# Kernel optimization log

Measured on AMD Instinct MI355X. Metric: run time of the kernel, lower is better.

The kernel has to match this reference:

```python
import jax, jax.numpy as jnp
import numpy as np


def setup_inputs() -> dict:
    key = jax.random.key(0)
    k1, k2, k3 = jax.random.split(key, 3)
    B, H, G, L, S, D = 2, 8, 4, 2048, 2048, 128
    q = jax.random.normal(k1, (B, H, G, L, D), dtype=jnp.float32)
    k = jax.random.normal(k2, (B, H, 1, S, D), dtype=jnp.float32)
    v = jax.random.normal(k3, (B, H, 1, S, D), dtype=jnp.float32)
    return {"q": q, "k": k, "v": v}


def reference(q, k, v):
    # q: [B,H,G,L,D]; k,v: [B,H,1,S,D] broadcast over G groups.
    # NOTE: original module does NOT scale by 1/sqrt(D).
    kk = jnp.squeeze(k, axis=2)  # [B,H,S,D]
    vv = jnp.squeeze(v, axis=2)  # [B,H,S,D]
    scores = jnp.einsum('bhgld,bhsd->bhgls', q, kk)  # [B,H,G,L,S]
    probs = jax.nn.softmax(scores, axis=-1)
    return jnp.einsum('bhgls,bhsd->bhgld', probs, vv)  # [B,H,G,L,D]
```

## Files before the change

kernel.cpp:

```cpp
#include <hip/hip_runtime.h>
#include <hip/hip_bf16.h>
#include <math.h>

typedef __bf16 bf16x8 __attribute__((ext_vector_type(8)));
typedef __bf16 bf16x4 __attribute__((ext_vector_type(4)));
typedef float  f32x4  __attribute__((ext_vector_type(4)));

constexpr int D   = 128;
constexpr int LQ  = 2048;
constexpr int SK  = 2048;
constexpr int BM  = 256;
constexpr int BN  = 64;
constexpr int NKV = 16;

__device__ __forceinline__ void load_lds16(const void* g, void* l) {
  __builtin_amdgcn_global_load_lds((const __attribute__((address_space(1))) unsigned*)g,
                                   (__attribute__((address_space(3))) unsigned*)l, 16, 0, 0);
}

__global__ __launch_bounds__(256) void conv_k(const float* __restrict__ k,
                                              __bf16* __restrict__ khi,
                                              __bf16* __restrict__ klo) {
  const size_t i = ((size_t)blockIdx.x * 256 + threadIdx.x) * 4;
  f32x4 a = *(const f32x4*)(k + i);
  bf16x4 hi, lo;
#pragma unroll
  for (int j = 0; j < 4; ++j) {
    hi[j] = (__bf16)a[j];
    lo[j] = (__bf16)(a[j] - (float)hi[j]);
  }
  *(bf16x4*)(khi + i) = hi;
  *(bf16x4*)(klo + i) = lo;
}

__global__ __launch_bounds__(256) void transpose_v(const float* __restrict__ v,
                                                   __bf16* __restrict__ vt) {
  const int b    = blockIdx.x;
  const int bh   = b >> 6;
  const int blk2 = b & 63;
  const int t    = threadIdx.x;
  const int s0   = (blk2 * 2 + (t >> 7)) * 16;
  const int d    = t & 127;
  const float* src = v + ((size_t)bh * SK + s0) * D + d;
  bf16x8 o0, o1;
#pragma unroll
  for (int j = 0; j < 8; ++j) o0[j] = (__bf16)src[j * D];
#pragma unroll
  for (int j = 0; j < 8; ++j) o1[j] = (__bf16)src[(8 + j) * D];
  __bf16* dst = vt + ((size_t)bh * D + d) * SK + s0;
  *(bf16x8*)dst = o0;
  *(bf16x8*)(dst + 8) = o1;
}

__global__ __launch_bounds__(512, 2)
void gqa_fwd(const float* __restrict__ qg, const __bf16* __restrict__ khi_g,
             const __bf16* __restrict__ klo_g, const __bf16* __restrict__ vt_g,
             float* __restrict__ outg)
{
  __shared__ alignas(16) __bf16 Kh[2][BN * D];
  __shared__ alignas(16) __bf16 Kl[2][BN * D];
  __shared__ alignas(16) __bf16 Vs[2][D * BN];

  const int bid   = blockIdx.x;
  const int xcd   = bid & 7;
  const int idx   = bid >> 3;
  const int bh    = 2 * xcd + (idx & 1);
  const int grp   = (idx >> 1) & 3;
  const int qtile = idx >> 3;
  const int bhg   = bh * 4 + grp;

  const int tid  = threadIdx.x;
  const int wave = tid >> 6;
  const int lane = tid & 63;
  const int i16  = lane & 15;
  const int quad = lane >> 4;

  const float*  qbase = qg + (size_t)bhg * (LQ * D) + (size_t)(qtile * BM) * D;
  const __bf16* khb   = khi_g + (size_t)bh * (SK * D);
  const __bf16* klb   = klo_g + (size_t)bh * (SK * D);
  const __bf16* vtb   = vt_g + (size_t)bh * (D * SK);

  auto stage = [&](int s0, int buf) {
#pragma unroll
    for (int c = 0; c < 2; ++c) {
      const int wc   = 2 * wave + c;
      const int srow = wc * 4 + (lane >> 4);
      const int jk   = (lane & 15) ^ (srow & 15);
      load_lds16(khb + (size_t)(s0 + srow) * D + 8 * jk, (char*)&Kh[buf][0] + wc * 1024);
      load_lds16(klb + (size_t)(s0 + srow) * D + 8 * jk, (char*)&Kl[buf][0] + wc * 1024);
      const int drow = wc * 8 + (lane >> 3);
      const int jv   = (lane & 7) ^ (drow & 7);
      load_lds16(vtb + (size_t)drow * SK + s0 + 8 * jv, (char*)&Vs[buf][0] + wc * 1024);
    }
  };

  stage(0, 0);

  bf16x8 qhi[2][4], qlo[2][4];
#pragma unroll
  for (int u = 0; u < 2; ++u) {
    const float* qp = qbase + (size_t)(32 * wave + 16 * u + i16) * D + 8 * quad;
#pragma unroll
    for (int t = 0; t < 4; ++t) {
      f32x4 a = *(const f32x4*)(qp + 32 * t);
      f32x4 b = *(const f32x4*)(qp + 32 * t + 4);
#pragma unroll
      for (int j = 0; j < 4; ++j) {
        qhi[u][t][j]     = (__bf16)a[j];
        qlo[u][t][j]     = (__bf16)(a[j] - (float)qhi[u][t][j]);
        qhi[u][t][j + 4] = (__bf16)b[j];
        qlo[u][t][j + 4] = (__bf16)(b[j] - (float)qhi[u][t][j + 4]);
      }
    }
  }

  f32x4 o_acc[2][8];
#pragma unroll
  for (int u = 0; u < 2; ++u)
#pragma unroll
    for (int c = 0; c < 8; ++c) o_acc[u][c] = (f32x4){0.f, 0.f, 0.f, 0.f};
  float m_r[2] = {-INFINITY, -INFINITY};
  float l_r[2] = {0.f, 0.f};

  asm volatile("s_waitcnt vmcnt(0)" ::: "memory");
  __syncthreads();

  for (int it = 0; it < SK / BN; ++it) {
    const int cur = it & 1;
    const __bf16* khc = &Kh[cur][0];
    const __bf16* klc = &Kl[cur][0];
    const __bf16* vsc = &Vs[cur][0];

    if (it + 1 < SK / BN) stage((it + 1) * BN, cur ^ 1);

    f32x4 sf[2][4];
#pragma unroll
    for (int u = 0; u < 2; ++u)
#pragma unroll
      for (int n = 0; n < 4; ++n) sf[u][n] = (f32x4){0.f, 0.f, 0.f, 0.f};
#pragma unroll
    for (int n = 0; n < 4; ++n) {
#pragma unroll
      for (int t = 0; t < 4; ++t) {
        const int ke = (16 * n + i16) * 128 + 8 * ((4 * t + quad) ^ i16);
        bf16x8 kh = *(const bf16x8*)&khc[ke];
        bf16x8 kl = *(const bf16x8*)&klc[ke];
#pragma unroll
        for (int u = 0; u < 2; ++u) {
          sf[u][n] = __builtin_amdgcn_mfma_f32_16x16x32_bf16(kh, qhi[u][t], sf[u][n], 0, 0, 0);
          sf[u][n] = __builtin_amdgcn_mfma_f32_16x16x32_bf16(kh, qlo[u][t], sf[u][n], 0, 0, 0);
          sf[u][n] = __builtin_amdgcn_mfma_f32_16x16x32_bf16(kl, qhi[u][t], sf[u][n], 0, 0, 0);
        }
      }
    }

    bf16x8 pb[2][2];
#pragma unroll
    for (int u = 0; u < 2; ++u) {
      float mx = sf[u][0][0];
#pragma unroll
      for (int n = 0; n < 4; ++n)
#pragma unroll
        for (int r = 0; r < 4; ++r) mx = fmaxf(mx, sf[u][n][r]);
      mx = fmaxf(mx, __shfl_xor(mx, 16, 64));
      mx = fmaxf(mx, __shfl_xor(mx, 32, 64));
      const float mnew  = fmaxf(m_r[u], mx);
      const float alpha = __expf(m_r[u] - mnew);
      m_r[u] = mnew;
      float rs = 0.f;
#pragma unroll
      for (int t = 0; t < 2; ++t) {
#pragma unroll
        for (int h = 0; h < 2; ++h) {
#pragma unroll
          for (int r = 0; r < 4; ++r) {
            const float p  = __expf(sf[u][2 * t + h][r] - mnew);
            const __bf16 pbv = (__bf16)p;
            pb[u][t][4 * h + r] = pbv;
            rs += (float)pbv;
          }
        }
      }
      rs += __shfl_xor(rs, 16, 64);
      rs += __shfl_xor(rs, 32, 64);
      l_r[u] = l_r[u] * alpha + rs;
#pragma unroll
      for (int c = 0; c < 8; ++c)
#pragma unroll
        for (int r = 0; r < 4; ++r) o_acc[u][c][r] *= alpha;
    }

#pragma unroll
    for (int c = 0; c < 8; ++c) {
      const int vbase = (16 * c + i16) * 64 + 4 * (quad & 1);
      const int xh    = i16 & 7;
#pragma unroll
      for (int t = 0; t < 2; ++t) {
        const int c0 = (4 * t + (quad >> 1)) ^ xh;
        const int c1 = (4 * t + 2 + (quad >> 1)) ^ xh;
        bf16x4 v0 = *(const bf16x4*)&vsc[vbase + 8 * c0];
        bf16x4 v1 = *(const bf16x4*)&vsc[vbase + 8 * c1];
        bf16x8 av = __builtin_shufflevector(v0, v1, 0, 1, 2, 3, 4, 5, 6, 7);
#pragma unroll
        for (int u = 0; u < 2; ++u)
          o_acc[u][c] = __builtin_amdgcn_mfma_f32_16x16x32_bf16(av, pb[u][t], o_acc[u][c], 0, 0, 0);
      }
    }

    asm volatile("s_waitcnt vmcnt(0)" ::: "memory");
    __syncthreads();
  }

  float* obase = outg + (size_t)bhg * (LQ * D) + (size_t)(qtile * BM) * D;
#pragma unroll
  for (int u = 0; u < 2; ++u) {
    const float inv = 1.f / l_r[u];
    float* op = obase + (size_t)(32 * wave + 16 * u + i16) * D;
#pragma unroll
    for (int c = 0; c < 8; ++c) {
      f32x4 r4 = o_acc[u][c] * inv;
      *(f32x4*)(op + 16 * c + 4 * quad) = r4;
    }
  }
}

extern "C" void kernel_launch(void* const* d_in, const int* in_sizes, int n_in,
                              void* d_out, int out_size, void* d_ws, size_t ws_size,
                              hipStream_t stream) {
  const float* q = (const float*)d_in[0];
  const float* k = (const float*)d_in[1];
  const float* v = (const float*)d_in[2];
  float* out = (float*)d_out;
  (void)in_sizes; (void)n_in; (void)out_size; (void)ws_size;

  const size_t kv_elems = (size_t)NKV * SK * D;
  __bf16* khi = (__bf16*)d_ws;
  __bf16* klo = khi + kv_elems;
  __bf16* vt  = klo + kv_elems;

  conv_k<<<dim3(kv_elems / (256 * 4)), 256, 0, stream>>>(k, khi, klo);
  transpose_v<<<dim3(NKV * 64), 256, 0, stream>>>(v, vt);
  gqa_fwd<<<dim3(8 * (LQ / BM) * 8), 512, 0, stream>>>(q, khi, klo, vt, out);
}
```

Measured before the change: 406.2 us.

## Single-buffer V with split K/V staging, lazy rescale, exp2 softmax, occupancy hint

K and V staging are split: V now uses a single LDS buffer loaded at the start of each iteration and waited on with a partial vmcnt before the PV MFMA, while K stays double-buffered. This cuts LDS use, and the launch bound is raised to target 4 blocks per CU. V is pre-permuted in the transpose kernel so the PV operand is one 16-byte LDS read instead of two 8-byte reads. Q is prescaled by log2e so the softmax can use exp2f, and the running max is only updated when a wave-wide threshold is exceeded, skipping the rescale. The lazy-max threshold lets unnormalized exponentials grow to about 2^11.5, which risks precision, and the extra K prefetch on the last iteration is wasted traffic.

```diff
diff --git a/kernel.cpp b/kernel.cpp
--- a/kernel.cpp
+++ b/kernel.cpp
@@ -12,6 +12,7 @@
 constexpr int BM  = 256;
 constexpr int BN  = 64;
 constexpr int NKV = 16;
+constexpr int NT  = SK / BN;
 
 __device__ __forceinline__ void load_lds16(const void* g, void* l) {
   __builtin_amdgcn_global_load_lds((const __attribute__((address_space(1))) unsigned*)g,
@@ -37,29 +38,37 @@
                                                    __bf16* __restrict__ vt) {
   const int b    = blockIdx.x;
   const int bh   = b >> 6;
-  const int blk2 = b & 63;
-  const int t    = threadIdx.x;
-  const int s0   = (blk2 * 2 + (t >> 7)) * 16;
-  const int d    = t & 127;
-  const float* src = v + ((size_t)bh * SK + s0) * D + d;
+  const int t2   = (b & 63) * 256 + threadIdx.x;
+  const int d    = t2 & 127;
+  const int slot = t2 >> 7;
+  const int G    = slot >> 1;
+  const int h2   = slot & 1;
+  const float* src = v + ((size_t)bh * SK + 32 * G) * D + d;
   bf16x8 o0, o1;
 #pragma unroll
-  for (int j = 0; j < 8; ++j) o0[j] = (__bf16)src[j * D];
-#pragma unroll
-  for (int j = 0; j < 8; ++j) o1[j] = (__bf16)src[(8 + j) * D];
-  __bf16* dst = vt + ((size_t)bh * D + d) * SK + s0;
+  for (int qq = 0; qq < 2; ++qq)
+#pragma unroll
+    for (int h = 0; h < 2; ++h)
+#pragma unroll
+      for (int r = 0; r < 4; ++r) {
+        const int idx = 8 * qq + 4 * h + r;
+        const int w   = 16 * h + 4 * (2 * h2 + qq) + r;
+        const __bf16 val = (__bf16)src[(size_t)w * D];
+        if (idx < 8) o0[idx] = val; else o1[idx - 8] = val;
+      }
+  __bf16* dst = vt + ((size_t)bh * D + d) * SK + 32 * G + 16 * h2;
   *(bf16x8*)dst = o0;
   *(bf16x8*)(dst + 8) = o1;
 }
 
-__global__ __launch_bounds__(512, 2)
+__global__ __launch_bounds__(512, 4)
 void gqa_fwd(const float* __restrict__ qg, const __bf16* __restrict__ khi_g,
              const __bf16* __restrict__ klo_g, const __bf16* __restrict__ vt_g,
              float* __restrict__ outg)
 {
   __shared__ alignas(16) __bf16 Kh[2][BN * D];
   __shared__ alignas(16) __bf16 Kl[2][BN * D];
-  __shared__ alignas(16) __bf16 Vs[2][D * BN];
+  __shared__ alignas(16) __bf16 Vs[D * BN];
 
   const int bid   = blockIdx.x;
   const int xcd   = bid & 7;
@@ -80,7 +89,7 @@
   const __bf16* klb   = klo_g + (size_t)bh * (SK * D);
   const __bf16* vtb   = vt_g + (size_t)bh * (D * SK);
 
-  auto stage = [&](int s0, int buf) {
+  auto stage_k = [&](int s0, int buf) {
 #pragma unroll
     for (int c = 0; c < 2; ++c) {
       const int wc   = 2 * wave + c;
@@ -88,14 +97,22 @@
       const int jk   = (lane & 15) ^ (srow & 15);
       load_lds16(khb + (size_t)(s0 + srow) * D + 8 * jk, (char*)&Kh[buf][0] + wc * 1024);
       load_lds16(klb + (size_t)(s0 + srow) * D + 8 * jk, (char*)&Kl[buf][0] + wc * 1024);
+    }
+  };
+  auto stage_v = [&](int s0) {
+#pragma unroll
+    for (int c = 0; c < 2; ++c) {
+      const int wc   = 2 * wave + c;
       const int drow = wc * 8 + (lane >> 3);
       const int jv   = (lane & 7) ^ (drow & 7);
-      load_lds16(vtb + (size_t)drow * SK + s0 + 8 * jv, (char*)&Vs[buf][0] + wc * 1024);
+      load_lds16(vtb + (size_t)drow * SK + s0 + 8 * jv, (char*)&Vs[0] + wc * 1024);
     }
   };
 
-  stage(0, 0);
-
+  stage_v(0);
+  stage_k(0, 0);
+
+  constexpr float LOG2E = 1.44269504089f;
   bf16x8 qhi[2][4], qlo[2][4];
 #pragma unroll
   for (int u = 0; u < 2; ++u) {
@@ -106,10 +123,12 @@
       f32x4 b = *(const f32x4*)(qp + 32 * t + 4);
 #pragma unroll
       for (int j = 0; j < 4; ++j) {
-        qhi[u][t][j]     = (__bf16)a[j];
-        qlo[u][t][j]     = (__bf16)(a[j] - (float)qhi[u][t][j]);
-        qhi[u][t][j + 4] = (__bf16)b[j];
-        qlo[u][t][j + 4] = (__bf16)(b[j] - (float)qhi[u][t][j + 4]);
+        const float a2 = a[j] * LOG2E;
+        const float b2 = b[j] * LOG2E;
+        qhi[u][t][j]     = (__bf16)a2;
+        qlo[u][t][j]     = (__bf16)(a2 - (float)qhi[u][t][j]);
+        qhi[u][t][j + 4] = (__bf16)b2;
+        qlo[u][t][j + 4] = (__bf16)(b2 - (float)qhi[u][t][j + 4]);
       }
     }
   }
@@ -125,13 +144,13 @@
   asm volatile("s_waitcnt vmcnt(0)" ::: "memory");
   __syncthreads();
 
-  for (int it = 0; it < SK / BN; ++it) {
+  for (int it = 0; it < NT; ++it) {
     const int cur = it & 1;
     const __bf16* khc = &Kh[cur][0];
     const __bf16* klc = &Kl[cur][0];
-    const __bf16* vsc = &Vs[cur][0];
-
-    if (it + 1 < SK / BN) stage((it + 1) * BN, cur ^ 1);
+
+    if (it > 0) stage_v(it * BN);
+    stage_k(((it + 1) & (NT - 1)) * BN, cur ^ 1);
 
     f32x4 sf[2][4];
 #pragma unroll
@@ -157,50 +176,48 @@
     bf16x8 pb[2][2];
 #pragma unroll
     for (int u = 0; u < 2; ++u) {
-      float mx = sf[u][0][0];
-#pragma unroll
-      for (int n = 0; n < 4; ++n)
-#pragma unroll
-        for (int r = 0; r < 4; ++r) mx = fmaxf(mx, sf[u][n][r]);
+      const float ma = fmaxf(fmaxf(sf[u][0][0], sf[u][0][1]), fmaxf(sf[u][0][2], sf[u][0][3]));
+      const float mb = fmaxf(fmaxf(sf[u][1][0], sf[u][1][1]), fmaxf(sf[u][1][2], sf[u][1][3]));
+      const float mc = fmaxf(fmaxf(sf[u][2][0], sf[u][2][1]), fmaxf(sf[u][2][2], sf[u][2][3]));
+      const float md = fmaxf(fmaxf(sf[u][3][0], sf[u][3][1]), fmaxf(sf[u][3][2], sf[u][3][3]));
+      float mx = fmaxf(fmaxf(ma, mb), fmaxf(mc, md));
       mx = fmaxf(mx, __shfl_xor(mx, 16, 64));
       mx = fmaxf(mx, __shfl_xor(mx, 32, 64));
-      const float mnew  = fmaxf(m_r[u], mx);
-      const float alpha = __expf(m_r[u] - mnew);
-      m_r[u] = mnew;
-      float rs = 0.f;
-#pragma unroll
-      for (int t = 0; t < 2; ++t) {
-#pragma unroll
-        for (int h = 0; h < 2; ++h) {
+      if (__any(mx > m_r[u] + 11.5f)) {
+        const float mnew  = fmaxf(m_r[u], mx);
+        const float alpha = exp2f(m_r[u] - mnew);
+        m_r[u] = mnew;
+        l_r[u] *= alpha;
+#pragma unroll
+        for (int c = 0; c < 8; ++c) o_acc[u][c] = o_acc[u][c] * alpha;
+      }
+      f32x4 rs4 = (f32x4){0.f, 0.f, 0.f, 0.f};
+#pragma unroll
+      for (int t = 0; t < 2; ++t)
+#pragma unroll
+        for (int h = 0; h < 2; ++h)
 #pragma unroll
           for (int r = 0; r < 4; ++r) {
-            const float p  = __expf(sf[u][2 * t + h][r] - mnew);
-            const __bf16 pbv = (__bf16)p;
-            pb[u][t][4 * h + r] = pbv;
-            rs += (float)pbv;
+            const float p   = exp2f(sf[u][2 * t + h][r] - m_r[u]);
+            const __bf16 pv = (__bf16)p;
+            pb[u][t][4 * h + r] = pv;
+            rs4[r] += (float)pv;
           }
-        }
-      }
+      float rs = (rs4[0] + rs4[1]) + (rs4[2] + rs4[3]);
       rs += __shfl_xor(rs, 16, 64);
       rs += __shfl_xor(rs, 32, 64);
-      l_r[u] = l_r[u] * alpha + rs;
-#pragma unroll
-      for (int c = 0; c < 8; ++c)
-#pragma unroll
-        for (int r = 0; r < 4; ++r) o_acc[u][c][r] *= alpha;
-    }
+      l_r[u] += rs;
+    }
+
+    asm volatile("s_waitcnt vmcnt(4)" ::: "memory");
+    __syncthreads();
 
 #pragma unroll
     for (int c = 0; c < 8; ++c) {
-      const int vbase = (16 * c + i16) * 64 + 4 * (quad & 1);
-      const int xh    = i16 & 7;
+      const int row = 16 * c + i16;
 #pragma unroll
       for (int t = 0; t < 2; ++t) {
-        const int c0 = (4 * t + (quad >> 1)) ^ xh;
-        const int c1 = (4 * t + 2 + (quad >> 1)) ^ xh;
-        bf16x4 v0 = *(const bf16x4*)&vsc[vbase + 8 * c0];
-        bf16x4 v1 = *(const bf16x4*)&vsc[vbase + 8 * c1];
-        bf16x8 av = __builtin_shufflevector(v0, v1, 0, 1, 2, 3, 4, 5, 6, 7);
+        bf16x8 av = *(const bf16x8*)&Vs[row * 64 + 8 * ((4 * t + quad) ^ (i16 & 7))];
 #pragma unroll
         for (int u = 0; u < 2; ++u)
           o_acc[u][c] = __builtin_amdgcn_mfma_f32_16x16x32_bf16(av, pb[u][t], o_acc[u][c], 0, 0, 0);
```

Result: slower. 1.093 ms (+169.0%).
